# Kernel optimization log

Measured on AMD Instinct MI355X. Metric: run time of the kernel, lower is better.

The kernel has to match this reference:

```python
import jax, jax.numpy as jnp
import numpy as np

HIDDEN = 1024
NUM_HEADS = 16
HEAD_DIM = HIDDEN // NUM_HEADS
B, S = 4, 4096


def setup_inputs() -> dict:
    key = jax.random.key(0)
    ks = jax.random.split(key, 7)
    scale = 1.0 / np.sqrt(HIDDEN)
    return {
        "hidden_states": jax.random.normal(ks[0], (B, S, HIDDEN), dtype=jnp.float32),
        "Wq": jax.random.normal(ks[1], (HIDDEN, HIDDEN), dtype=jnp.float32) * scale,
        "bq": jax.random.normal(ks[2], (HIDDEN,), dtype=jnp.float32) * 0.01,
        "Wk": jax.random.normal(ks[3], (HIDDEN, HIDDEN), dtype=jnp.float32) * scale,
        "bk": jax.random.normal(ks[4], (HIDDEN,), dtype=jnp.float32) * 0.01,
        "Wv": jax.random.normal(ks[5], (HIDDEN, HIDDEN), dtype=jnp.float32) * scale,
        "bv": jax.random.normal(ks[6], (HIDDEN,), dtype=jnp.float32) * 0.01,
    }


def _split_heads(x):
    # [B, S, H*D] -> [B, H, S, D]
    b, s, _ = x.shape
    return x.reshape(b, s, NUM_HEADS, HEAD_DIM).transpose(0, 2, 1, 3)


def reference(hidden_states, Wq, bq, Wk, bk, Wv, bv):
    # Fused-style QKV: single stacked GEMM, then split + reshape to heads.
    Wqkv = jnp.concatenate([Wq, Wk, Wv], axis=1)          # [H, 3H]
    bqkv = jnp.concatenate([bq, bk, bv], axis=0)           # [3H]
    qkv = jnp.einsum("bsh,hf->bsf", hidden_states, Wqkv) + bqkv  # [B, S, 3H]
    q, k, v = jnp.split(qkv, 3, axis=-1)
    return (_split_heads(q), _split_heads(k), _split_heads(v))
```

## Files before the change

### kernel.cpp

```cpp
#include <hip/hip_runtime.h>
#include <hip/hip_bf16.h>


#define M_TOT 16384
#define N_TOT 3072
#define K_TOT 1024

typedef __bf16 bf16x8 __attribute__((ext_vector_type(8)));
typedef float f32x16 __attribute__((ext_vector_type(16)));

#define AS1(p) ((const __attribute__((address_space(1))) void*)(p))
#define AS3(p) ((__attribute__((address_space(3))) void*)(p))

__device__ __forceinline__ unsigned short f2bf(float f) {
    unsigned int u = __builtin_bit_cast(unsigned int, f);
    u += 0x7fffu + ((u >> 16) & 1u);
    return (unsigned short)(u >> 16);
}

__global__ void convert_hidden(const float* __restrict__ x,
                               unsigned short* __restrict__ y, int n4) {
    int i = blockIdx.x * blockDim.x + threadIdx.x;
    int stride = gridDim.x * blockDim.x;
    for (; i < n4; i += stride) {
        float4 v = ((const float4*)x)[i];
        ushort4 o;
        o.x = f2bf(v.x); o.y = f2bf(v.y); o.z = f2bf(v.z); o.w = f2bf(v.w);
        ((ushort4*)y)[i] = o;
    }
}

__global__ void convert_weights(const float* __restrict__ Wq,
                                const float* __restrict__ Wk,
                                const float* __restrict__ Wv,
                                unsigned short* __restrict__ Bt) {
    __shared__ unsigned short tile[64][65];
    const float* W = (blockIdx.z == 0) ? Wq : (blockIdx.z == 1) ? Wk : Wv;
    int k0 = blockIdx.y * 64;
    int f0 = blockIdx.x * 64;
    int tx = threadIdx.x & 63;
    int ty = threadIdx.x >> 6;
#pragma unroll
    for (int r = 0; r < 16; ++r) {
        int k = ty + r * 4;
        tile[k][tx] = f2bf(W[(size_t)(k0 + k) * 1024 + f0 + tx]);
    }
    __syncthreads();
#pragma unroll
    for (int r = 0; r < 16; ++r) {
        int fr = ty + r * 4;
        Bt[(size_t)(blockIdx.z * 1024 + f0 + fr) * 1024 + k0 + tx] = tile[tx][fr];
    }
}

__launch_bounds__(512, 2)
__global__ void qkv_gemm(const unsigned short* __restrict__ A,
                         const unsigned short* __restrict__ Bt,
                         const float* __restrict__ bq,
                         const float* __restrict__ bk,
                         const float* __restrict__ bv,
                         float* __restrict__ out) {
    __shared__ __align__(16) unsigned short As[2][16384];
    __shared__ __align__(16) unsigned short Bs[2][16384];

    const int tid  = threadIdx.x;
    const int wave = tid >> 6;
    const int lane = tid & 63;
    const int r5   = lane & 31;
    const int half = lane >> 5;
    const int swr  = r5 & 7;

    const int xcd = blockIdx.x & 7;
    const int j   = blockIdx.x >> 3;
    const int jm  = j & 7;
    const int jn  = j >> 3;

    const int wr = wave >> 2;
    const int wc = wave & 3;

    const int trow = tid >> 3;
    const int tkq8 = ((tid & 7) ^ (trow & 7)) * 8;

    int st = xcd * 3;
    int bm = (st & 7) * 8 + jm;
    int bn = (st >> 3) * 4 + jn;
    const unsigned short* gA = A  + (size_t)(bm * 256 + trow) * 1024 + tkq8;
    const unsigned short* gB = Bt + (size_t)(bn * 256 + trow) * 1024 + tkq8;

#define STAGE(c)                                                                \
    do {                                                                        \
        __builtin_amdgcn_global_load_lds(AS1(sA + (size_t)(c)*65536),           \
                                         AS3(dA + ((c)*512 + wave * 64) * 8),   \
                                         16, 0, 0);                             \
        __builtin_amdgcn_global_load_lds(AS1(sB + (size_t)(c)*65536),           \
                                         AS3(dB + ((c)*512 + wave * 64) * 8),   \
                                         16, 0, 0);                             \
    } while (0)

    {
        const unsigned short* sA = gA;
        const unsigned short* sB = gB;
        unsigned short* dA = (unsigned short*)As[0];
        unsigned short* dB = (unsigned short*)Bs[0];
#pragma unroll
        for (int c = 0; c < 4; ++c) STAGE(c);
    }

    for (int i = 0; i < 3; ++i) {
        int bm2 = bm, bn2 = bn;
        const unsigned short *gA2 = gA, *gB2 = gB;
        if (i < 2) {
            int st2 = xcd * 3 + i + 1;
            bm2 = (st2 & 7) * 8 + jm;
            bn2 = (st2 >> 3) * 4 + jn;
            gA2 = A  + (size_t)(bm2 * 256 + trow) * 1024 + tkq8;
            gB2 = Bt + (size_t)(bn2 * 256 + trow) * 1024 + tkq8;
        }

        f32x16 acc[4][2] = {};

#pragma unroll 2
        for (int t = 0; t < 16; ++t) {
            const int cur = t & 1;
            const unsigned short* Ab = As[cur];
            const unsigned short* Bb = Bs[cur];
            unsigned short* dA = (unsigned short*)As[cur ^ 1];
            unsigned short* dB = (unsigned short*)Bs[cur ^ 1];
            const bool stg = (t < 15) || (i < 2);
            const unsigned short* sA = (t < 15) ? gA + (size_t)(t + 1) * 64 : gA2;
            const unsigned short* sB = (t < 15) ? gB + (size_t)(t + 1) * 64 : gB2;

#pragma unroll
            for (int ks = 0; ks < 4; ++ks) {
                bf16x8 av[4], bvv[2];
                const int prd = ((ks * 2 + half) ^ swr) * 8;
                if (ks == 0) {
                    if (stg) {
                        STAGE(0);
                        asm volatile("s_waitcnt vmcnt(2)" ::: "memory");
                    } else {
                        asm volatile("s_waitcnt vmcnt(0)" ::: "memory");
                    }
                    __builtin_amdgcn_s_barrier();
                    __builtin_amdgcn_sched_barrier(0);
#pragma unroll
                    for (int ib = 0; ib < 4; ++ib)
                        av[ib] = *(const bf16x8*)&Ab[(wr * 128 + ib * 32 + r5) * 64 + prd];
#pragma unroll
                    for (int jb = 0; jb < 2; ++jb)
                        bvv[jb] = *(const bf16x8*)&Bb[(wc * 64 + jb * 32 + r5) * 64 + prd];
                } else {
#pragma unroll
                    for (int ib = 0; ib < 4; ++ib)
                        av[ib] = *(const bf16x8*)&Ab[(wr * 128 + ib * 32 + r5) * 64 + prd];
#pragma unroll
                    for (int jb = 0; jb < 2; ++jb)
                        bvv[jb] = *(const bf16x8*)&Bb[(wc * 64 + jb * 32 + r5) * 64 + prd];
                    if (stg) STAGE(ks);
                }
                asm volatile("s_waitcnt lgkmcnt(0)" ::: "memory");
                __builtin_amdgcn_sched_barrier(0);
                __builtin_amdgcn_s_setprio(1);
#pragma unroll
                for (int ib = 0; ib < 4; ++ib)
#pragma unroll
                    for (int jb = 0; jb < 2; ++jb)
                        acc[ib][jb] = __builtin_amdgcn_mfma_f32_32x32x16_bf16(
                            av[ib], bvv[jb], acc[ib][jb], 0, 0, 0);
                __builtin_amdgcn_s_setprio(0);
            }
            __builtin_amdgcn_s_barrier();
        }

        {
            const int section = bn >> 2;
            const int nloc0   = (bn & 3) * 256 + wc * 64;
            const float* bias = (section == 0) ? bq : (section == 1) ? bk : bv;
            float* outsec = out + (size_t)section * (4u * 16u * 4096u * 64u);

#pragma unroll
            for (int jb = 0; jb < 2; ++jb) {
                int f = nloc0 + jb * 32 + r5;
                float bval = bias[f];
                int h = f >> 6, d = f & 63;
                size_t hb = (size_t)h * (4096u * 64u);
#pragma unroll
                for (int ib = 0; ib < 4; ++ib) {
                    int mbase = bm * 256 + wr * 128 + ib * 32 + 4 * half;
#pragma unroll
                    for (int reg = 0; reg < 16; ++reg) {
                        int m = mbase + (reg & 3) + 8 * (reg >> 2);
                        int b = m >> 12, s = m & 4095;
                        outsec[(size_t)b * (16u * 4096u * 64u) + hb + (size_t)s * 64u + d] =
                            acc[ib][jb][reg] + bval;
                    }
                }
            }
        }

        bm = bm2; bn = bn2; gA = gA2; gB = gB2;
    }
#undef STAGE
}

extern "C" void kernel_launch(void* const* d_in, const int* in_sizes, int n_in,
                              void* d_out, int out_size, void* d_ws, size_t ws_size,
                              hipStream_t stream) {
    const float* hs = (const float*)d_in[0];
    const float* Wq = (const float*)d_in[1];
    const float* bq = (const float*)d_in[2];
    const float* Wk = (const float*)d_in[3];
    const float* bk = (const float*)d_in[4];
    const float* Wv = (const float*)d_in[5];
    const float* bv = (const float*)d_in[6];
    float* out = (float*)d_out;

    unsigned short* Abf  = (unsigned short*)d_ws;
    unsigned short* Btbf = Abf + (size_t)M_TOT * K_TOT;

    convert_hidden<<<2048, 256, 0, stream>>>(hs, Abf, (M_TOT * K_TOT) / 4);
    convert_weights<<<dim3(16, 16, 3), 256, 0, stream>>>(Wq, Wk, Wv, Btbf);
    qkv_gemm<<<256, 512, 0, stream>>>(Abf, Btbf, bq, bk, bv, out);
}
```

Before: 372.1 us.

## Switch GEMM LDS pipeline to four-slot ring of 32-wide K chunks

Splits the shared-memory staging from two 64-wide K buffers into a four-slot ring of 32-wide K chunks, prefetching up to three chunks ahead with vmcnt-based waits, and adjusts the XOR swizzle to the narrower row. The aim is deeper overlap between global-to-LDS loads and MFMA work, so the barrier waits expose less memory latency. In exchange there are twice as many barriers per K step, and the new swizzle may change the LDS bank-conflict pattern.

```diff
diff --git a/kernel.cpp b/kernel.cpp
--- a/kernel.cpp
+++ b/kernel.cpp
@@ -60,15 +60,15 @@
                          const float* __restrict__ bk,
                          const float* __restrict__ bv,
                          float* __restrict__ out) {
-    __shared__ __align__(16) unsigned short As[2][16384];
-    __shared__ __align__(16) unsigned short Bs[2][16384];
+    __shared__ __align__(16) unsigned short As[4][8192];
+    __shared__ __align__(16) unsigned short Bs[4][8192];
 
     const int tid  = threadIdx.x;
     const int wave = tid >> 6;
     const int lane = tid & 63;
     const int r5   = lane & 31;
     const int half = lane >> 5;
-    const int swr  = r5 & 7;
+    const int sw2  = (r5 >> 1) & 3;
 
     const int xcd = blockIdx.x & 7;
     const int j   = blockIdx.x >> 3;
@@ -78,33 +78,57 @@
     const int wr = wave >> 2;
     const int wc = wave & 3;
 
-    const int trow = tid >> 3;
-    const int tkq8 = ((tid & 7) ^ (trow & 7)) * 8;
+    const int tr = tid >> 2;
+    const int kq = (tid & 3) ^ ((tid >> 3) & 3);
+    const size_t gOff = (size_t)tr * 1024 + (size_t)kq * 8;
 
     int st = xcd * 3;
     int bm = (st & 7) * 8 + jm;
     int bn = (st >> 3) * 4 + jn;
-    const unsigned short* gA = A  + (size_t)(bm * 256 + trow) * 1024 + tkq8;
-    const unsigned short* gB = Bt + (size_t)(bn * 256 + trow) * 1024 + tkq8;
-
-#define STAGE(c)                                                                \
+    const unsigned short* gA = A  + (size_t)bm * 256 * 1024;
+    const unsigned short* gB = Bt + (size_t)bn * 256 * 1024;
+
+#define STAGE(slot, koff, bA, bB)                                               \
     do {                                                                        \
-        __builtin_amdgcn_global_load_lds(AS1(sA + (size_t)(c)*65536),           \
-                                         AS3(dA + ((c)*512 + wave * 64) * 8),   \
+        const unsigned short* sA_ = (bA) + (size_t)(koff) + gOff;               \
+        const unsigned short* sB_ = (bB) + (size_t)(koff) + gOff;               \
+        unsigned short* dA_ = &As[(slot)][wave * 512];                          \
+        unsigned short* dB_ = &Bs[(slot)][wave * 512];                          \
+        __builtin_amdgcn_global_load_lds(AS1(sA_), AS3(dA_), 16, 0, 0);         \
+        __builtin_amdgcn_global_load_lds(AS1(sA_ + 131072), AS3(dA_ + 4096),    \
                                          16, 0, 0);                             \
-        __builtin_amdgcn_global_load_lds(AS1(sB + (size_t)(c)*65536),           \
-                                         AS3(dB + ((c)*512 + wave * 64) * 8),   \
+        __builtin_amdgcn_global_load_lds(AS1(sB_), AS3(dB_), 16, 0, 0);         \
+        __builtin_amdgcn_global_load_lds(AS1(sB_ + 131072), AS3(dB_ + 4096),    \
                                          16, 0, 0);                             \
     } while (0)
 
-    {
-        const unsigned short* sA = gA;
-        const unsigned short* sB = gB;
-        unsigned short* dA = (unsigned short*)As[0];
-        unsigned short* dB = (unsigned short*)Bs[0];
-#pragma unroll
-        for (int c = 0; c < 4; ++c) STAGE(c);
-    }
+#define PAIR(slotc)                                                             \
+    do {                                                                        \
+        const unsigned short* Au = &As[(slotc)][0];                             \
+        const unsigned short* Bu = &Bs[(slotc)][0];                             \
+        _Pragma("unroll") for (int ks = 0; ks < 2; ++ks) {                      \
+            bf16x8 av[4], bvv[2];                                               \
+            const int po = ((ks * 2 + half) ^ sw2) * 8;                         \
+            _Pragma("unroll") for (int ib = 0; ib < 4; ++ib)                    \
+                av[ib] = *(const bf16x8*)&Au[(wr * 128 + ib * 32 + r5) * 32 + po]; \
+            _Pragma("unroll") for (int jb = 0; jb < 2; ++jb)                    \
+                bvv[jb] = *(const bf16x8*)&Bu[(wc * 64 + jb * 32 + r5) * 32 + po]; \
+            asm volatile("s_waitcnt lgkmcnt(0)" ::: "memory");                  \
+            __builtin_amdgcn_sched_barrier(0);                                  \
+            __builtin_amdgcn_s_setprio(1);                                      \
+            _Pragma("unroll") for (int ib = 0; ib < 4; ++ib)                    \
+                _Pragma("unroll") for (int jb = 0; jb < 2; ++jb)                \
+                    acc[ib][jb] = __builtin_amdgcn_mfma_f32_32x32x16_bf16(      \
+                        av[ib], bvv[jb], acc[ib][jb], 0, 0, 0);                 \
+            __builtin_amdgcn_s_setprio(0);                                      \
+        }                                                                       \
+    } while (0)
+
+#define UKOFF(u) ((size_t)(((u) >> 1) * 64 + ((u) & 1) * 32))
+
+    STAGE(0, UKOFF(0), gA, gB);
+    STAGE(1, UKOFF(1), gA, gB);
+    STAGE(2, UKOFF(2), gA, gB);
 
     for (int i = 0; i < 3; ++i) {
         int bm2 = bm, bn2 = bn;
@@ -113,63 +137,40 @@
             int st2 = xcd * 3 + i + 1;
             bm2 = (st2 & 7) * 8 + jm;
             bn2 = (st2 >> 3) * 4 + jn;
-            gA2 = A  + (size_t)(bm2 * 256 + trow) * 1024 + tkq8;
-            gB2 = Bt + (size_t)(bn2 * 256 + trow) * 1024 + tkq8;
+            gA2 = A  + (size_t)bm2 * 256 * 1024;
+            gB2 = Bt + (size_t)bn2 * 256 * 1024;
         }
+        const bool lastIter = (i == 2);
 
         f32x16 acc[4][2] = {};
 
 #pragma unroll 2
         for (int t = 0; t < 16; ++t) {
-            const int cur = t & 1;
-            const unsigned short* Ab = As[cur];
-            const unsigned short* Bb = Bs[cur];
-            unsigned short* dA = (unsigned short*)As[cur ^ 1];
-            unsigned short* dB = (unsigned short*)Bs[cur ^ 1];
-            const bool stg = (t < 15) || (i < 2);
-            const unsigned short* sA = (t < 15) ? gA + (size_t)(t + 1) * 64 : gA2;
-            const unsigned short* sB = (t < 15) ? gB + (size_t)(t + 1) * 64 : gB2;
-
-#pragma unroll
-            for (int ks = 0; ks < 4; ++ks) {
-                bf16x8 av[4], bvv[2];
-                const int prd = ((ks * 2 + half) ^ swr) * 8;
-                if (ks == 0) {
-                    if (stg) {
-                        STAGE(0);
-                        asm volatile("s_waitcnt vmcnt(2)" ::: "memory");
-                    } else {
-                        asm volatile("s_waitcnt vmcnt(0)" ::: "memory");
-                    }
-                    __builtin_amdgcn_s_barrier();
-                    __builtin_amdgcn_sched_barrier(0);
-#pragma unroll
-                    for (int ib = 0; ib < 4; ++ib)
-                        av[ib] = *(const bf16x8*)&Ab[(wr * 128 + ib * 32 + r5) * 64 + prd];
-#pragma unroll
-                    for (int jb = 0; jb < 2; ++jb)
-                        bvv[jb] = *(const bf16x8*)&Bb[(wc * 64 + jb * 32 + r5) * 64 + prd];
-                } else {
-#pragma unroll
-                    for (int ib = 0; ib < 4; ++ib)
-                        av[ib] = *(const bf16x8*)&Ab[(wr * 128 + ib * 32 + r5) * 64 + prd];
-#pragma unroll
-                    for (int jb = 0; jb < 2; ++jb)
-                        bvv[jb] = *(const bf16x8*)&Bb[(wc * 64 + jb * 32 + r5) * 64 + prd];
-                    if (stg) STAGE(ks);
-                }
-                asm volatile("s_waitcnt lgkmcnt(0)" ::: "memory");
-                __builtin_amdgcn_sched_barrier(0);
-                __builtin_amdgcn_s_setprio(1);
-#pragma unroll
-                for (int ib = 0; ib < 4; ++ib)
-#pragma unroll
-                    for (int jb = 0; jb < 2; ++jb)
-                        acc[ib][jb] = __builtin_amdgcn_mfma_f32_32x32x16_bf16(
-                            av[ib], bvv[jb], acc[ib][jb], 0, 0, 0);
-                __builtin_amdgcn_s_setprio(0);
+            if (lastIter && t == 15)
+                asm volatile("s_waitcnt vmcnt(4)" ::: "memory");
+            else
+                asm volatile("s_waitcnt vmcnt(8)" ::: "memory");
+            __builtin_amdgcn_s_barrier();
+            __builtin_amdgcn_sched_barrier(0);
+            {
+                const int u = 2 * t + 3;
+                if (u < 32)        STAGE(u & 3, UKOFF(u), gA, gB);
+                else if (i < 2)    STAGE((u - 32) & 3, UKOFF(u - 32), gA2, gB2);
             }
+            PAIR((2 * t) & 3);
+
+            if (lastIter && t == 15)
+                asm volatile("s_waitcnt vmcnt(0)" ::: "memory");
+            else
+                asm volatile("s_waitcnt vmcnt(8)" ::: "memory");
             __builtin_amdgcn_s_barrier();
+            __builtin_amdgcn_sched_barrier(0);
+            {
+                const int u = 2 * t + 4;
+                if (u < 32)        STAGE(u & 3, UKOFF(u), gA, gB);
+                else if (i < 2)    STAGE((u - 32) & 3, UKOFF(u - 32), gA2, gB2);
+            }
+            PAIR((2 * t + 1) & 3);
         }
 
         {
@@ -201,6 +202,8 @@
         bm = bm2; bn = bn2; gA = gA2; gB = gB2;
     }
 #undef STAGE
+#undef PAIR
+#undef UKOFF
 }
 
 extern "C" void kernel_launch(void* const* d_in, const int* in_sizes, int n_in,
```

Result: no change. 370.4 us (-0.5%).
